# Performance work log

Measured on AMD Instinct MI355X. Metric: run time of the kernel, lower is better.

Reference implementation:

```python
import jax, jax.numpy as jnp
import numpy as np

D_MODEL = 2048
NUM_HEADS = 16
HEAD_DIM = D_MODEL // NUM_HEADS
D_FF = 4 * D_MODEL
B, L = 2, 2048
LN_EPS = 1e-6


def layer_norm(x, scale, bias):
    x32 = x.astype(jnp.float32)
    mu = jnp.mean(x32, axis=-1, keepdims=True)
    var = jnp.mean(jnp.square(x32 - mu), axis=-1, keepdims=True)
    return (x32 - mu) * jax.lax.rsqrt(var + LN_EPS) * scale + bias


def setup_inputs() -> dict:
    key = jax.random.key(0)
    ks = jax.random.split(key, 10)
    s = 1.0 / np.sqrt(D_MODEL)
    x = jax.random.normal(ks[0], (B, L, D_MODEL), dtype=jnp.float32)
    mask = jnp.tril(jnp.ones((L, L), dtype=bool))[None, None, :, :]  # causal [1,1,L,L]
    wq = jax.random.normal(ks[1], (D_MODEL, D_MODEL), jnp.float32) * s
    wk = jax.random.normal(ks[2], (D_MODEL, D_MODEL), jnp.float32) * s
    wv = jax.random.normal(ks[3], (D_MODEL, D_MODEL), jnp.float32) * s
    wo = jax.random.normal(ks[4], (D_MODEL, D_MODEL), jnp.float32) * s
    w1 = jax.random.normal(ks[5], (D_MODEL, D_FF), jnp.float32) * s
    b1 = jnp.zeros((D_FF,), jnp.float32)
    w2 = jax.random.normal(ks[6], (D_FF, D_MODEL), jnp.float32) * (1.0 / np.sqrt(D_FF))
    b2 = jnp.zeros((D_MODEL,), jnp.float32)
    ln1_scale = jnp.ones((D_MODEL,), jnp.float32)
    ln1_bias = jnp.zeros((D_MODEL,), jnp.float32)
    ln2_scale = jnp.ones((D_MODEL,), jnp.float32)
    ln2_bias = jnp.zeros((D_MODEL,), jnp.float32)
    return {"x": x, "mask": mask, "ln1_scale": ln1_scale, "ln1_bias": ln1_bias,
            "wq": wq, "wk": wk, "wv": wv, "wo": wo,
            "ln2_scale": ln2_scale, "ln2_bias": ln2_bias,
            "w1": w1, "b1": b1, "w2": w2, "b2": b2}


def reference(x, mask, ln1_scale, ln1_bias, wq, wk, wv, wo,
              ln2_scale, ln2_bias, w1, b1, w2, b2):
    residual = x
    h = layer_norm(x, ln1_scale, ln1_bias)
    b, l, _ = h.shape
    q = (h @ wq).reshape(b, l, NUM_HEADS, HEAD_DIM)
    k = (h @ wk).reshape(b, l, NUM_HEADS, HEAD_DIM)
    v = (h @ wv).reshape(b, l, NUM_HEADS, HEAD_DIM)
    scores = jnp.einsum('bqhd,bkhd->bhqk', q, k) / jnp.sqrt(jnp.float32(HEAD_DIM))
    scores = jnp.where(mask, scores, -100000.0)
    attn = jax.nn.softmax(scores, axis=-1)
    attn_out = jnp.einsum('bhqk,bkhd->bqhd', attn, v).reshape(b, l, D_MODEL)
    x = residual + attn_out @ wo
    mlp = jax.nn.gelu(layer_norm(x, ln2_scale, ln2_bias) @ w1 + b1)
    return x + mlp @ w2 + b2
```

## Files before the change

kernel.cpp:

```cpp
#include <hip/hip_runtime.h>
#include <hip/hip_bf16.h>

typedef unsigned short u16;
typedef __bf16 bf16x8 __attribute__((ext_vector_type(8)));
typedef float f32x4 __attribute__((ext_vector_type(4)));

#define D_MODEL 2048
#define D_FF    8192
#define NH      16
#define HD      128
#define BATCH   2
#define SEQ     2048
#define ROWS    (BATCH*SEQ)

__device__ __forceinline__ u16 f2bf(float f) {
  union { __hip_bfloat16 h; u16 u; } cv;
  cv.h = __float2bfloat16(f);
  return cv.u;
}

__device__ __forceinline__ void gload16(const u16* g, u16* l) {
  __builtin_amdgcn_global_load_lds((const __attribute__((address_space(1))) void*)g,
                                   (__attribute__((address_space(3))) void*)l,
                                   16, 0, 0);
}

__device__ __forceinline__ float gelu_f(float x) {
  const float k0 = 0.7978845608028654f, k1 = 0.044715f;
  return 0.5f * x * (1.0f + tanhf(k0 * (x + k1 * x * x * x)));
}

__global__ __launch_bounds__(256) void ln_bf16_kernel(
    const float* __restrict__ x, const float* __restrict__ sc,
    const float* __restrict__ bs, u16* __restrict__ out)
{
  __shared__ float red[8];
  const int row = blockIdx.x, t = threadIdx.x;
  const int w = t >> 6, l = t & 63;
  const float* xr = x + (size_t)row * D_MODEL;
  float4 a = ((const float4*)xr)[t*2];
  float4 b = ((const float4*)xr)[t*2+1];
  float s  = a.x+a.y+a.z+a.w + b.x+b.y+b.z+b.w;
  float s2 = a.x*a.x+a.y*a.y+a.z*a.z+a.w*a.w + b.x*b.x+b.y*b.y+b.z*b.z+b.w*b.w;
  for (int off = 32; off; off >>= 1) { s += __shfl_down(s, off); s2 += __shfl_down(s2, off); }
  if (l == 0) { red[w] = s; red[4+w] = s2; }
  __syncthreads();
  s  = red[0]+red[1]+red[2]+red[3];
  s2 = red[4]+red[5]+red[6]+red[7];
  const float mu  = s * (1.0f / D_MODEL);
  const float var = s2 * (1.0f / D_MODEL) - mu * mu;
  const float inv = rsqrtf(var + 1e-6f);
  float4 g0 = ((const float4*)sc)[t*2], g1 = ((const float4*)sc)[t*2+1];
  float4 q0 = ((const float4*)bs)[t*2], q1 = ((const float4*)bs)[t*2+1];
  union { u16 u[8]; uint4 v; } o;
  o.u[0] = f2bf((a.x-mu)*inv*g0.x + q0.x);
  o.u[1] = f2bf((a.y-mu)*inv*g0.y + q0.y);
  o.u[2] = f2bf((a.z-mu)*inv*g0.z + q0.z);
  o.u[3] = f2bf((a.w-mu)*inv*g0.w + q0.w);
  o.u[4] = f2bf((b.x-mu)*inv*g1.x + q1.x);
  o.u[5] = f2bf((b.y-mu)*inv*g1.y + q1.y);
  o.u[6] = f2bf((b.z-mu)*inv*g1.z + q1.z);
  o.u[7] = f2bf((b.w-mu)*inv*g1.w + q1.w);
  *(uint4*)(&out[(size_t)row * D_MODEL + t*8]) = o.v;
}

__global__ __launch_bounds__(256) void transpose_w(
    const float* __restrict__ in, u16* __restrict__ out, int R, int C)
{
  __shared__ float tile[64][65];
  const int t = threadIdx.x;
  const int c0 = blockIdx.x*64, r0 = blockIdx.y*64;
  const int cq = (t & 15) * 4, rb = t >> 4;
#pragma unroll
  for (int i = 0; i < 4; ++i) {
    const float4 v = *(const float4*)&in[(size_t)(r0 + rb + i*16)*C + c0 + cq];
    tile[rb + i*16][cq+0] = v.x; tile[rb + i*16][cq+1] = v.y;
    tile[rb + i*16][cq+2] = v.z; tile[rb + i*16][cq+3] = v.w;
  }
  __syncthreads();
#pragma unroll
  for (int i = 0; i < 4; ++i) {
    const int oc = rb + i*16;
    ushort4 o;
    o.x = f2bf(tile[cq+0][oc]); o.y = f2bf(tile[cq+1][oc]);
    o.z = f2bf(tile[cq+2][oc]); o.w = f2bf(tile[cq+3][oc]);
    *(ushort4*)&out[(size_t)(c0 + oc)*R + r0 + cq] = o;
  }
}

__global__ __launch_bounds__(256) void transpose_v(
    const u16* __restrict__ qkv, u16* __restrict__ vt)
{
  __shared__ u16 tile[32][34];
  const int t = threadIdx.x;
  const int b = blockIdx.z;
  const int c0 = blockIdx.x*32, r0 = blockIdx.y*32;
  const int col = t & 31, rb = t >> 5;
  const u16* inb = qkv + (size_t)b*SEQ*3*D_MODEL + 2*D_MODEL;
#pragma unroll
  for (int i = 0; i < 4; ++i)
    tile[rb+i*8][col] = inb[(size_t)(r0+rb+i*8)*(3*D_MODEL) + c0+col];
  __syncthreads();
  u16* ob = vt + (size_t)b*SEQ*D_MODEL;
#pragma unroll
  for (int i = 0; i < 4; ++i)
    ob[(size_t)(c0+rb+i*8)*SEQ + r0+col] = tile[col][rb+i*8];
}

template<int EPI, int BNP>
__global__ __launch_bounds__(512, 1) void gemm8p(
    const u16* __restrict__ A, const u16* __restrict__ BT,
    void* __restrict__ Cout, const float* __restrict__ bias,
    const float* __restrict__ res, int N, int K, int gridN)
{
  constexpr int GB    = BNP / 128;
  constexpr int NI    = BNP / 64;
  constexpr int BHALF = BNP * 32;
  constexpr int BUFU  = 16384 + BNP * 64;
  __shared__ __align__(16) u16 lds[2 * BUFU];
  const int t = threadIdx.x;
  const int nwg = gridDim.x;
  const int wg = (int)blockIdx.x;
  const int wgid = (wg & 7) * (nwg >> 3) + (wg >> 3);
  const int bx = wgid % gridN, by = wgid / gridN;
  const int m0 = by * 256, n0 = bx * BNP;
  const int w = t >> 6, l = t & 63;
  const int wm = w >> 2, wn = w & 3;
  const int l15 = l & 15, lq = l >> 4;

  const int srow = t >> 2;
  const int c0s  = (t & 3) ^ ((srow >> 1) & 3);
  const u16* aS0 = A  + (size_t)(m0 + srow) * K + c0s * 8;
  const u16* aS1 = A  + (size_t)(m0 + 128 + srow) * K + c0s * 8;
  const u16* bS0 = BT + (size_t)(n0 + srow) * K + c0s * 8;
  const u16* bS1 = BT + (size_t)(n0 + (GB == 2 ? 128 : 0) + srow) * K + c0s * 8;

  int offA_[2][4], offB_[NI];
#pragma unroll
  for (int mq = 0; mq < 2; ++mq)
#pragma unroll
    for (int i2 = 0; i2 < 4; ++i2) {
      const int ra = wm * 128 + mq * 64 + i2 * 16 + l15;
      offA_[mq][i2] = ra * 32 + ((lq ^ ((ra >> 1) & 3)) * 8);
    }
#pragma unroll
  for (int j = 0; j < NI; ++j) {
    const int rb = wn * (BNP / 4) + j * 16 + l15;
    offB_[j] = rb * 32 + ((lq ^ ((rb >> 1) & 3)) * 8);
  }

  f32x4 acc[8][NI] = {};
  bf16x8 bfv[NI];
  const int nt = K >> 6;

#define STAGE_A(dst, Tn, kh) { \
    gload16(aS0 + (size_t)(Tn)*64 + (kh)*32, (dst) + (kh)*8192 + t*8); \
    gload16(aS1 + (size_t)(Tn)*64 + (kh)*32, (dst) + (kh)*8192 + 4096 + t*8); }
#define STAGE_B(dst, Tn, kh) { \
    gload16(bS0 + (size_t)(Tn)*64 + (kh)*32, (dst) + 16384 + (kh)*BHALF + t*8); \
    if (GB == 2) gload16(bS1 + (size_t)(Tn)*64 + (kh)*32, (dst) + 16384 + (kh)*BHALF + 4096 + t*8); }
#define VMS { if (GB == 2) { asm volatile("s_waitcnt vmcnt(4)" ::: "memory"); } \
              else        { asm volatile("s_waitcnt vmcnt(3)" ::: "memory"); } \
              __builtin_amdgcn_sched_barrier(0); }
#define VM0 { asm volatile("s_waitcnt vmcnt(0)" ::: "memory"); __builtin_amdgcn_sched_barrier(0); }
#define NOP { }

#define PHASE(bufc, MQ, KH, DOB, STAGECODE, WAITCODE) { \
    bf16x8 af_[4]; \
    _Pragma("unroll") \
    for (int i2 = 0; i2 < 4; ++i2) \
      af_[i2] = *(const bf16x8*)&(bufc)[offA_[MQ][i2] + (KH)*8192]; \
    if (DOB) { \
      _Pragma("unroll") \
      for (int j = 0; j < NI; ++j) \
        bfv[j] = *(const bf16x8*)&(bufc)[offB_[j] + 16384 + (KH)*BHALF]; \
    } \
    STAGECODE; \
    __builtin_amdgcn_s_barrier(); \
    asm volatile("s_waitcnt lgkmcnt(0)" ::: "memory"); \
    __builtin_amdgcn_sched_barrier(0); \
    __builtin_amdgcn_s_setprio(1); \
    _Pragma("unroll") \
    for (int i2 = 0; i2 < 4; ++i2) \
      _Pragma("unroll") \
      for (int j = 0; j < NI; ++j) \
        acc[(MQ)*4 + i2][j] = __builtin_amdgcn_mfma_f32_16x16x32_bf16(af_[i2], bfv[j], acc[(MQ)*4 + i2][j], 0, 0, 0); \
    __builtin_amdgcn_s_setprio(0); \
    WAITCODE; \
    __builtin_amdgcn_s_barrier(); }

  {
    u16* b0p = lds;
    STAGE_A(b0p, 0, 0); STAGE_B(b0p, 0, 0); STAGE_A(b0p, 0, 1); STAGE_B(b0p, 0, 1);
  }
  VMS;
  __builtin_amdgcn_s_barrier();

  for (int T = 0; T < nt - 1; ++T) {
    u16* bufc = &lds[(T & 1) * BUFU];
    u16* bufn = &lds[((T + 1) & 1) * BUFU];
    PHASE(bufc, 0, 0, 1, STAGE_A(bufn, T + 1, 0), NOP);
    PHASE(bufc, 1, 0, 0, STAGE_B(bufn, T + 1, 0), VMS);
    PHASE(bufc, 0, 1, 1, STAGE_A(bufn, T + 1, 1), NOP);
    PHASE(bufc, 1, 1, 0, STAGE_B(bufn, T + 1, 1), VMS);
  }
  {
    u16* bufc = &lds[((nt - 1) & 1) * BUFU];
    PHASE(bufc, 0, 0, 1, NOP, NOP);
    PHASE(bufc, 1, 0, 0, NOP, VM0);
    PHASE(bufc, 0, 1, 1, NOP, NOP);
    PHASE(bufc, 1, 1, 0, NOP, NOP);
  }
#undef PHASE
#undef STAGE_A
#undef STAGE_B
#undef VMS
#undef VM0
#undef NOP

  const int rowb = m0 + wm * 128;
  const int colb = n0 + wn * (BNP / 4);
#pragma unroll
  for (int mi = 0; mi < 8; ++mi) {
#pragma unroll
    for (int ni = 0; ni < NI; ++ni) {
      const int col = colb + ni * 16 + l15;
      const int row0 = rowb + mi * 16 + lq * 4;
      float bv = (EPI == 2 || EPI == 3) ? bias[col] : 0.f;
#pragma unroll
      for (int r = 0; r < 4; ++r) {
        const float v = acc[mi][ni][r];
        const size_t idx = (size_t)(row0 + r) * N + col;
        if (EPI == 0)      ((u16*)Cout)[idx] = f2bf(v);
        else if (EPI == 1) ((float*)Cout)[idx] = v + res[idx];
        else if (EPI == 2) ((u16*)Cout)[idx] = f2bf(gelu_f(v + bv));
        else               ((float*)Cout)[idx] = v + bv + res[idx];
      }
    }
  }
}

__global__ __launch_bounds__(256) void attn_kernel(
    const u16* __restrict__ qkv, const u16* __restrict__ vt,
    u16* __restrict__ out)
{
  __shared__ u16 Ks[64*128];
  __shared__ u16 Vs[128*64];
  __shared__ u16 Ps[4*16*64];
  const int t = threadIdx.x;
  const int pairi = blockIdx.x & 15, bh = blockIdx.x >> 4;
  const int b = bh >> 4, h = bh & 15;
  const int w = t >> 6, l = t & 63;
  const int l15 = l & 15, lq = l >> 4;
  const size_t kbase = (size_t)b*SEQ*(3*D_MODEL) + D_MODEL + h*HD;
  const size_t vbase = (size_t)(b*SEQ + h*HD) * SEQ;
  u16* pw = &Ps[w*1024];

  for (int qsel = 0; qsel < 2; ++qsel) {
    const int qt = qsel ? (31 - pairi) : pairi;

    bf16x8 qf[4];
    {
      const u16* qb = qkv + (size_t)(b*SEQ + qt*64 + w*16 + l15)*(3*D_MODEL) + h*HD;
#pragma unroll
      for (int kk = 0; kk < 4; ++kk)
        qf[kk] = *(const bf16x8*)(qb + kk*32 + lq*8);
    }
    float m[4]    = {-INFINITY, -INFINITY, -INFINITY, -INFINITY};
    float lsum[4] = {0.f, 0.f, 0.f, 0.f};
    f32x4 acc_o[8] = {};

    for (int j = 0; j <= qt; ++j) {
      __syncthreads();
#pragma unroll
      for (int i = 0; i < 4; ++i) {
        const int o16 = i*256 + t;
        {
          const int row = o16 >> 4, cs = o16 & 15;
          const int srcc = cs ^ (row & 7);
          gload16(qkv + kbase + (size_t)(j*64+row)*(3*D_MODEL) + srcc*8, &Ks[o16*8]);
        }
        {
          const int row = o16 >> 3, cs = o16 & 7;
          const int srcc = cs ^ (row & 7);
          gload16(vt + vbase + (size_t)row*SEQ + j*64 + srcc*8, &Vs[o16*8]);
        }
      }
      __syncthreads();

      f32x4 sacc[4] = {};
#pragma unroll
      for (int nf = 0; nf < 4; ++nf) {
        const int kr = nf*16 + l15;
        const int sw = kr & 7;
#pragma unroll
        for (int kk = 0; kk < 4; ++kk) {
          bf16x8 kf = *(const bf16x8*)&Ks[kr*128 + ((kk*4+lq) ^ sw)*8];
          sacc[nf] = __builtin_amdgcn_mfma_f32_16x16x32_bf16(qf[kk], kf, sacc[nf], 0, 0, 0);
        }
      }

      const float scale = 0.08838834764831845f;
      if (j == qt) {
#pragma unroll
        for (int nf = 0; nf < 4; ++nf)
#pragma unroll
          for (int r = 0; r < 4; ++r) {
            float s = sacc[nf][r] * scale;
            const int ki = nf*16 + l15;
            const int qi = w*16 + lq*4 + r;
            if (ki > qi) s = -100000.0f;
            sacc[nf][r] = s;
          }
      } else {
#pragma unroll
        for (int nf = 0; nf < 4; ++nf)
#pragma unroll
          for (int r = 0; r < 4; ++r) sacc[nf][r] *= scale;
      }

      float scal[4];
#pragma unroll
      for (int r = 0; r < 4; ++r) {
        float mx = fmaxf(fmaxf(sacc[0][r], sacc[1][r]), fmaxf(sacc[2][r], sacc[3][r]));
#pragma unroll
        for (int off = 1; off < 16; off <<= 1)
          mx = fmaxf(mx, __shfl_xor(mx, off));
        const float mn = fmaxf(m[r], mx);
        scal[r] = __expf(m[r] - mn);
        m[r] = mn;
        float rs = 0.f;
#pragma unroll
        for (int nf = 0; nf < 4; ++nf) {
          const float p = __expf(sacc[nf][r] - mn);
          sacc[nf][r] = p;
          rs += p;
        }
#pragma unroll
        for (int off = 1; off < 16; off <<= 1)
          rs += __shfl_xor(rs, off);
        lsum[r] = lsum[r]*scal[r] + rs;
      }
#pragma unroll
      for (int nf2 = 0; nf2 < 8; ++nf2)
#pragma unroll
        for (int r = 0; r < 4; ++r) acc_o[nf2][r] *= scal[r];

#pragma unroll
      for (int nf = 0; nf < 4; ++nf)
#pragma unroll
        for (int r = 0; r < 4; ++r) {
          const int qr = lq*4 + r, kc = nf*16 + l15;
          pw[qr*64 + (((kc>>3) ^ (qr&7))*8 + (kc&7))] = f2bf(sacc[nf][r]);
        }

#pragma unroll
      for (int kk2 = 0; kk2 < 2; ++kk2) {
        bf16x8 pf = *(const bf16x8*)&pw[l15*64 + (((kk2*4+lq) ^ (l15&7))*8)];
#pragma unroll
        for (int nf2 = 0; nf2 < 8; ++nf2) {
          const int vr = nf2*16 + l15;
          bf16x8 vf = *(const bf16x8*)&Vs[vr*64 + ((kk2*4+lq) ^ (vr&7))*8];
          acc_o[nf2] = __builtin_amdgcn_mfma_f32_16x16x32_bf16(pf, vf, acc_o[nf2], 0, 0, 0);
        }
      }
    }

    const size_t ro = (size_t)(b*SEQ + qt*64 + w*16 + lq*4);
#pragma unroll
    for (int r = 0; r < 4; ++r) {
      const float inv = 1.0f / lsum[r];
#pragma unroll
      for (int nf2 = 0; nf2 < 8; ++nf2)
        out[(ro + r)*D_MODEL + h*HD + nf2*16 + l15] = f2bf(acc_o[nf2][r] * inv);
    }
    __syncthreads();
  }
}

extern "C" void kernel_launch(void* const* d_in, const int* in_sizes, int n_in,
                              void* d_out, int out_size, void* d_ws, size_t ws_size,
                              hipStream_t stream)
{
  (void)in_sizes; (void)n_in; (void)out_size; (void)ws_size;
  const float* x    = (const float*)d_in[0];
  const float* ln1s = (const float*)d_in[2];
  const float* ln1b = (const float*)d_in[3];
  const float* wq   = (const float*)d_in[4];
  const float* wk   = (const float*)d_in[5];
  const float* wv   = (const float*)d_in[6];
  const float* wo   = (const float*)d_in[7];
  const float* ln2s = (const float*)d_in[8];
  const float* ln2b = (const float*)d_in[9];
  const float* w1   = (const float*)d_in[10];
  const float* b1   = (const float*)d_in[11];
  const float* w2   = (const float*)d_in[12];
  const float* b2   = (const float*)d_in[13];
  float* out = (float*)d_out;

  char* ws = (char*)d_ws;
  constexpr size_t OFF_WQKV = 0;
  constexpr size_t OFF_WO   = OFF_WQKV + (size_t)3*D_MODEL*D_MODEL*2;
  constexpr size_t OFF_W1   = OFF_WO   + (size_t)D_MODEL*D_MODEL*2;
  constexpr size_t OFF_W2   = OFF_W1   + (size_t)D_FF*D_MODEL*2;
  constexpr size_t OFF_H    = OFF_W2   + (size_t)D_MODEL*D_FF*2;
  constexpr size_t OFF_QKV  = OFF_H    + (size_t)ROWS*D_MODEL*2;
  constexpr size_t OFF_VT   = OFF_QKV  + (size_t)ROWS*3*D_MODEL*2;
  constexpr size_t OFF_ATTN = OFF_VT   + (size_t)ROWS*D_MODEL*2;
  constexpr size_t OFF_X2   = OFF_ATTN + (size_t)ROWS*D_MODEL*2;

  u16*   wqkv_bt = (u16*)(ws + OFF_WQKV);
  u16*   wo_bt   = (u16*)(ws + OFF_WO);
  u16*   w1_bt   = (u16*)(ws + OFF_W1);
  u16*   w2_bt   = (u16*)(ws + OFF_W2);
  u16*   h_bf    = (u16*)(ws + OFF_H);
  u16*   qkv     = (u16*)(ws + OFF_QKV);
  u16*   vt      = (u16*)(ws + OFF_VT);
  u16*   act     = qkv;
  u16*   attn    = (u16*)(ws + OFF_ATTN);
  float* x2      = (float*)(ws + OFF_X2);

  const dim3 B256(256), B512(512);

  transpose_w<<<dim3(32,32),  B256, 0, stream>>>(wq, wqkv_bt,                 D_MODEL, D_MODEL);
  transpose_w<<<dim3(32,32),  B256, 0, stream>>>(wk, wqkv_bt + (size_t)D_MODEL*D_MODEL,   D_MODEL, D_MODEL);
  transpose_w<<<dim3(32,32),  B256, 0, stream>>>(wv, wqkv_bt + (size_t)2*D_MODEL*D_MODEL, D_MODEL, D_MODEL);
  transpose_w<<<dim3(32,32),  B256, 0, stream>>>(wo, wo_bt, D_MODEL, D_MODEL);
  transpose_w<<<dim3(128,32), B256, 0, stream>>>(w1, w1_bt, D_MODEL, D_FF);
  transpose_w<<<dim3(32,128), B256, 0, stream>>>(w2, w2_bt, D_FF, D_MODEL);

  ln_bf16_kernel<<<ROWS, B256, 0, stream>>>(x, ln1s, ln1b, h_bf);
  gemm8p<0,128><<<dim3(768), B512, 0, stream>>>(h_bf, wqkv_bt, qkv, nullptr, nullptr, 3*D_MODEL, D_MODEL, 48);
  transpose_v<<<dim3(64,64,2), B256, 0, stream>>>(qkv, vt);
  attn_kernel<<<dim3(BATCH*NH*16), B256, 0, stream>>>(qkv, vt, attn);
  gemm8p<1,128><<<dim3(256), B512, 0, stream>>>(attn, wo_bt, (void*)x2, nullptr, x, D_MODEL, D_MODEL, 16);
  ln_bf16_kernel<<<ROWS, B256, 0, stream>>>(x2, ln2s, ln2b, h_bf);
  gemm8p<2,256><<<dim3(512), B512, 0, stream>>>(h_bf, w1_bt, act, b1, nullptr, D_FF, D_MODEL, 32);
  gemm8p<3,128><<<dim3(256), B512, 0, stream>>>(act, w2_bt, (void*)out, b2, x2, D_MODEL, D_FF, 16);
}
```

Baseline: 666.1 us.

## Deepen GEMM prefetch pipeline and batch four weight transposes into one launch

The GEMM main loop now prefetches half of tile T+2 into the current buffer while computing tile T, which deepens the global-to-LDS pipeline and adds a separate epilogue iteration for the last two tiles. This is meant to hide more global load latency behind MFMA work. Separately, the four square weight transposes are merged into one launch with a z-dimension to cut kernel launch overhead. The buffer reuse within an iteration is intricate and risks a race if the wait and barrier placement is wrong.

```diff
diff --git a/kernel.cpp b/kernel.cpp
--- a/kernel.cpp
+++ b/kernel.cpp
@@ -88,6 +88,36 @@
   }
 }
 
+__global__ __launch_bounds__(256) void transpose_w4(
+    const float* __restrict__ s0, const float* __restrict__ s1,
+    const float* __restrict__ s2, const float* __restrict__ s3,
+    u16* __restrict__ d0, u16* __restrict__ d1,
+    u16* __restrict__ d2, u16* __restrict__ d3)
+{
+  __shared__ float tile[64][65];
+  const int z = blockIdx.z;
+  const float* in = (z == 0) ? s0 : (z == 1) ? s1 : (z == 2) ? s2 : s3;
+  u16* out       = (z == 0) ? d0 : (z == 1) ? d1 : (z == 2) ? d2 : d3;
+  const int t = threadIdx.x;
+  const int c0 = blockIdx.x*64, r0 = blockIdx.y*64;
+  const int cq = (t & 15) * 4, rb = t >> 4;
+#pragma unroll
+  for (int i = 0; i < 4; ++i) {
+    const float4 v = *(const float4*)&in[(size_t)(r0 + rb + i*16)*D_MODEL + c0 + cq];
+    tile[rb + i*16][cq+0] = v.x; tile[rb + i*16][cq+1] = v.y;
+    tile[rb + i*16][cq+2] = v.z; tile[rb + i*16][cq+3] = v.w;
+  }
+  __syncthreads();
+#pragma unroll
+  for (int i = 0; i < 4; ++i) {
+    const int oc = rb + i*16;
+    ushort4 o;
+    o.x = f2bf(tile[cq+0][oc]); o.y = f2bf(tile[cq+1][oc]);
+    o.z = f2bf(tile[cq+2][oc]); o.w = f2bf(tile[cq+3][oc]);
+    *(ushort4*)&out[(size_t)(c0 + oc)*D_MODEL + r0 + cq] = o;
+  }
+}
+
 __global__ __launch_bounds__(256) void transpose_v(
     const u16* __restrict__ qkv, u16* __restrict__ vt)
 {
@@ -191,23 +221,33 @@
 
   {
     u16* b0p = lds;
+    u16* b1p = &lds[BUFU];
     STAGE_A(b0p, 0, 0); STAGE_B(b0p, 0, 0); STAGE_A(b0p, 0, 1); STAGE_B(b0p, 0, 1);
+    STAGE_A(b1p, 1, 0); STAGE_B(b1p, 1, 0);
   }
   VMS;
   __builtin_amdgcn_s_barrier();
 
-  for (int T = 0; T < nt - 1; ++T) {
+  for (int T = 0; T < nt - 2; ++T) {
     u16* bufc = &lds[(T & 1) * BUFU];
     u16* bufn = &lds[((T + 1) & 1) * BUFU];
-    PHASE(bufc, 0, 0, 1, STAGE_A(bufn, T + 1, 0), NOP);
-    PHASE(bufc, 1, 0, 0, STAGE_B(bufn, T + 1, 0), VMS);
-    PHASE(bufc, 0, 1, 1, STAGE_A(bufn, T + 1, 1), NOP);
-    PHASE(bufc, 1, 1, 0, STAGE_B(bufn, T + 1, 1), VMS);
+    PHASE(bufc, 0, 0, 1, STAGE_A(bufn, T + 1, 1), NOP);
+    PHASE(bufc, 1, 0, 0, STAGE_B(bufn, T + 1, 1), VMS);
+    PHASE(bufc, 0, 1, 1, STAGE_A(bufc, T + 2, 0), NOP);
+    PHASE(bufc, 1, 1, 0, STAGE_B(bufc, T + 2, 0), NOP);
+  }
+  {
+    u16* bufc = &lds[((nt - 2) & 1) * BUFU];
+    u16* bufn = &lds[((nt - 1) & 1) * BUFU];
+    PHASE(bufc, 0, 0, 1, STAGE_A(bufn, nt - 1, 1), NOP);
+    PHASE(bufc, 1, 0, 0, STAGE_B(bufn, nt - 1, 1), VMS);
+    PHASE(bufc, 0, 1, 1, NOP, NOP);
+    PHASE(bufc, 1, 1, 0, NOP, VM0);
   }
   {
     u16* bufc = &lds[((nt - 1) & 1) * BUFU];
     PHASE(bufc, 0, 0, 1, NOP, NOP);
-    PHASE(bufc, 1, 0, 0, NOP, VM0);
+    PHASE(bufc, 1, 0, 0, NOP, NOP);
     PHASE(bufc, 0, 1, 1, NOP, NOP);
     PHASE(bufc, 1, 1, 0, NOP, NOP);
   }
@@ -422,10 +462,9 @@
 
   const dim3 B256(256), B512(512);
 
-  transpose_w<<<dim3(32,32),  B256, 0, stream>>>(wq, wqkv_bt,                 D_MODEL, D_MODEL);
-  transpose_w<<<dim3(32,32),  B256, 0, stream>>>(wk, wqkv_bt + (size_t)D_MODEL*D_MODEL,   D_MODEL, D_MODEL);
-  transpose_w<<<dim3(32,32),  B256, 0, stream>>>(wv, wqkv_bt + (size_t)2*D_MODEL*D_MODEL, D_MODEL, D_MODEL);
-  transpose_w<<<dim3(32,32),  B256, 0, stream>>>(wo, wo_bt, D_MODEL, D_MODEL);
+  transpose_w4<<<dim3(32,32,4), B256, 0, stream>>>(
+      wq, wk, wv, wo,
+      wqkv_bt, wqkv_bt + (size_t)D_MODEL*D_MODEL, wqkv_bt + (size_t)2*D_MODEL*D_MODEL, wo_bt);
   transpose_w<<<dim3(128,32), B256, 0, stream>>>(w1, w1_bt, D_MODEL, D_FF);
   transpose_w<<<dim3(32,128), B256, 0, stream>>>(w2, w2_bt, D_FF, D_MODEL);
 
```

Result: faster. 649.8 us, median of 2 (-2.5%).

## Deepen GEMM prefetch pipeline and merge weight transposes into one launch

Applied to the files above, without the earlier changes.

The GEMM main loop now prefetches half of tile T+2 into the current buffer while still computing on it, so global loads run further ahead of the MFMA work. A new epilogue section drains the extra stage, and one vmcnt wait per iteration is dropped. Separately, the six weight-transpose launches are merged into a single kernel that picks the source and destination from the block index, which cuts launch overhead. The reuse of the current buffer while it is being read depends on the order of phases and barriers, and gets this wrong would corrupt data.

```diff
diff --git a/kernel.cpp b/kernel.cpp
--- a/kernel.cpp
+++ b/kernel.cpp
@@ -64,12 +64,30 @@
   *(uint4*)(&out[(size_t)row * D_MODEL + t*8]) = o.v;
 }
 
-__global__ __launch_bounds__(256) void transpose_w(
-    const float* __restrict__ in, u16* __restrict__ out, int R, int C)
+__global__ __launch_bounds__(256) void transpose_all(
+    const float* __restrict__ wq, const float* __restrict__ wk,
+    const float* __restrict__ wv, const float* __restrict__ wo,
+    const float* __restrict__ w1, const float* __restrict__ w2,
+    u16* __restrict__ wqkv_bt, u16* __restrict__ wo_bt,
+    u16* __restrict__ w1_bt, u16* __restrict__ w2_bt)
 {
   __shared__ float tile[64][65];
+  const int id = (int)blockIdx.x;
+  const float* in; u16* out; int R, C, tx, ty;
+  if (id < 4096) {
+    const int z = id >> 10, tid = id & 1023;
+    in  = (z == 0) ? wq : (z == 1) ? wk : (z == 2) ? wv : wo;
+    out = (z == 3) ? wo_bt : wqkv_bt + (size_t)z * D_MODEL * D_MODEL;
+    R = D_MODEL; C = D_MODEL; tx = tid & 31; ty = tid >> 5;
+  } else if (id < 8192) {
+    const int tid = id - 4096;
+    in = w1; out = w1_bt; R = D_MODEL; C = D_FF; tx = tid & 127; ty = tid >> 7;
+  } else {
+    const int tid = id - 8192;
+    in = w2; out = w2_bt; R = D_FF; C = D_MODEL; tx = tid & 31; ty = tid >> 5;
+  }
   const int t = threadIdx.x;
-  const int c0 = blockIdx.x*64, r0 = blockIdx.y*64;
+  const int c0 = tx*64, r0 = ty*64;
   const int cq = (t & 15) * 4, rb = t >> 4;
 #pragma unroll
   for (int i = 0; i < 4; ++i) {
@@ -191,23 +209,33 @@
 
   {
     u16* b0p = lds;
+    u16* b1p = &lds[BUFU];
     STAGE_A(b0p, 0, 0); STAGE_B(b0p, 0, 0); STAGE_A(b0p, 0, 1); STAGE_B(b0p, 0, 1);
+    STAGE_A(b1p, 1, 0); STAGE_B(b1p, 1, 0);
   }
   VMS;
   __builtin_amdgcn_s_barrier();
 
-  for (int T = 0; T < nt - 1; ++T) {
+  for (int T = 0; T < nt - 2; ++T) {
     u16* bufc = &lds[(T & 1) * BUFU];
     u16* bufn = &lds[((T + 1) & 1) * BUFU];
-    PHASE(bufc, 0, 0, 1, STAGE_A(bufn, T + 1, 0), NOP);
-    PHASE(bufc, 1, 0, 0, STAGE_B(bufn, T + 1, 0), VMS);
-    PHASE(bufc, 0, 1, 1, STAGE_A(bufn, T + 1, 1), NOP);
-    PHASE(bufc, 1, 1, 0, STAGE_B(bufn, T + 1, 1), VMS);
+    PHASE(bufc, 0, 0, 1, STAGE_A(bufn, T + 1, 1), NOP);
+    PHASE(bufc, 1, 0, 0, STAGE_B(bufn, T + 1, 1), VMS);
+    PHASE(bufc, 0, 1, 1, STAGE_A(bufc, T + 2, 0), NOP);
+    PHASE(bufc, 1, 1, 0, STAGE_B(bufc, T + 2, 0), NOP);
+  }
+  {
+    u16* bufc = &lds[((nt - 2) & 1) * BUFU];
+    u16* bufn = &lds[((nt - 1) & 1) * BUFU];
+    PHASE(bufc, 0, 0, 1, STAGE_A(bufn, nt - 1, 1), NOP);
+    PHASE(bufc, 1, 0, 0, STAGE_B(bufn, nt - 1, 1), VMS);
+    PHASE(bufc, 0, 1, 1, NOP, NOP);
+    PHASE(bufc, 1, 1, 0, NOP, VM0);
   }
   {
     u16* bufc = &lds[((nt - 1) & 1) * BUFU];
     PHASE(bufc, 0, 0, 1, NOP, NOP);
-    PHASE(bufc, 1, 0, 0, NOP, VM0);
+    PHASE(bufc, 1, 0, 0, NOP, NOP);
     PHASE(bufc, 0, 1, 1, NOP, NOP);
     PHASE(bufc, 1, 1, 0, NOP, NOP);
   }
@@ -422,12 +450,8 @@
 
   const dim3 B256(256), B512(512);
 
-  transpose_w<<<dim3(32,32),  B256, 0, stream>>>(wq, wqkv_bt,                 D_MODEL, D_MODEL);
-  transpose_w<<<dim3(32,32),  B256, 0, stream>>>(wk, wqkv_bt + (size_t)D_MODEL*D_MODEL,   D_MODEL, D_MODEL);
-  transpose_w<<<dim3(32,32),  B256, 0, stream>>>(wv, wqkv_bt + (size_t)2*D_MODEL*D_MODEL, D_MODEL, D_MODEL);
-  transpose_w<<<dim3(32,32),  B256, 0, stream>>>(wo, wo_bt, D_MODEL, D_MODEL);
-  transpose_w<<<dim3(128,32), B256, 0, stream>>>(w1, w1_bt, D_MODEL, D_FF);
-  transpose_w<<<dim3(32,128), B256, 0, stream>>>(w2, w2_bt, D_FF, D_MODEL);
+  transpose_all<<<dim3(12288), B256, 0, stream>>>(
+      wq, wk, wv, wo, w1, w2, wqkv_bt, wo_bt, w1_bt, w2_bt);
 
   ln_bf16_kernel<<<ROWS, B256, 0, stream>>>(x, ln1s, ln1b, h_bf);
   gemm8p<0,128><<<dim3(768), B512, 0, stream>>>(h_bf, wqkv_bt, qkv, nullptr, nullptr, 3*D_MODEL, D_MODEL, 48);
```

New measurement: 642.0 us (median of 2 runs). 1.04x faster.
